# Performance work log

Hardware: AMD Instinct MI355X
Metric: run time of the kernel (lower is better)

The kernel has to match this reference:

```python
import jax, jax.numpy as jnp
import numpy as np

INPUT_DIM = 1024
OUTPUT_DIM = 1024


def setup_inputs() -> dict:
    key = jax.random.key(0)
    k1, k2, k3, k4 = jax.random.split(key, 4)
    B, S, D = 4, 2048, INPUT_DIM
    src = jax.random.normal(k1, (B, S, D), dtype=jnp.float32)
    tgt = jax.random.normal(k2, (B, S, D), dtype=jnp.float32)
    # nn.Linear(input_dim*2, output_dim): weight [out, in], bias [out]
    bound = 1.0 / np.sqrt(2 * D)
    W = jax.random.uniform(k3, (OUTPUT_DIM, 2 * D), jnp.float32, -bound, bound)
    b = jax.random.uniform(k4, (OUTPUT_DIM,), jnp.float32, -bound, bound)
    return {"src": src, "tgt": tgt, "W": W, "b": b}


def reference(src, tgt, W, b):
    # weight = bmm(tgt, src^T): [B, S_tgt, S_src]
    weight = jnp.einsum("btd,bsd->bts", tgt, src)
    # NOTE: original uses Softmax(dim=1) -> normalizes over the tgt axis
    weight = jax.nn.softmax(weight, axis=1)
    # weighted sum over src positions: [B, S_tgt, D]
    weight_sum = jnp.einsum("bts,bsd->btd", weight, src)
    output = jnp.concatenate([weight_sum, tgt], axis=2)  # [B, S_tgt, 2D]
    output = output @ W.T + b  # [B, S_tgt, output_dim]
    return (output, weight)
```

## Files before the change

### kernel.cpp

```cpp
#include <hip/hip_runtime.h>
#include <stdint.h>


#define B_   4
#define S_   2048
#define D_   1024
#define OUTD 1024

typedef unsigned short ushort_t;
typedef _Float16 half8 __attribute__((ext_vector_type(8)));
typedef float    f32x4 __attribute__((ext_vector_type(4)));

__device__ __forceinline__ ushort_t f2h(float f) {
    union { _Float16 h; ushort_t u; } v;
    v.h = (_Float16)f;
    return v.u;
}
__device__ __forceinline__ float h2f(ushort_t u) {
    union { _Float16 h; ushort_t u; } v;
    v.u = u;
    return (float)v.h;
}

__device__ __forceinline__ void ld16(const ushort_t* g, ushort_t* l) {
    __builtin_amdgcn_global_load_lds(
        (const __attribute__((address_space(1))) void*)g,
        (__attribute__((address_space(3))) void*)l, 16, 0, 0);
}


__global__ void k_split(const float4* __restrict__ src, const float4* __restrict__ tgt,
                        ushort4* __restrict__ sh,
                        ushort4* __restrict__ th, ushort4* __restrict__ tl)
{
    const int64_t n4 = (int64_t)B_ * S_ * D_ / 4;
    for (int64_t i = (int64_t)blockIdx.x * blockDim.x + threadIdx.x; i < n4;
         i += (int64_t)gridDim.x * blockDim.x) {
        float4 s = src[i];
        sh[i] = (ushort4){f2h(s.x), f2h(s.y), f2h(s.z), f2h(s.w)};
        float4 tv = tgt[i];
        ushort4 ht = {f2h(tv.x), f2h(tv.y), f2h(tv.z), f2h(tv.w)};
        th[i] = ht;
        tl[i] = (ushort4){f2h(tv.x - h2f(ht.x)), f2h(tv.y - h2f(ht.y)),
                          f2h(tv.z - h2f(ht.z)), f2h(tv.w - h2f(ht.w))};
    }
}

__global__ void k_wconv(const float4* __restrict__ W, ushort4* __restrict__ wb)
{
    const int64_t n4 = (int64_t)OUTD * 2 * D_ / 4;
    for (int64_t i = (int64_t)blockIdx.x * blockDim.x + threadIdx.x; i < n4;
         i += (int64_t)gridDim.x * blockDim.x) {
        float4 w = W[i];
        wb[i] = (ushort4){f2h(w.x), f2h(w.y), f2h(w.z), f2h(w.w)};
    }
}

__launch_bounds__(512, 2)
__global__ void k_gemm_logits(const ushort_t* __restrict__ Ah, const ushort_t* __restrict__ Al,
                              const ushort_t* __restrict__ Bs,
                              float* __restrict__ C,
                              float* __restrict__ pm, float* __restrict__ ps)
{
    const int M = S_, N = S_, K = D_;
    int b = blockIdx.z;
    Ah += (int64_t)b * M * K;  Al += (int64_t)b * M * K;
    Bs += (int64_t)b * N * K;
    C  += (int64_t)b * M * N;

    __shared__ __align__(16) ushort_t lds[3 * 24576];
    __shared__ float red_m[4][256], red_s[4][256];

    int t    = threadIdx.x;
    int m0   = blockIdx.y * 256, n0 = blockIdx.x * 256;
    int wave = t >> 6, lane = t & 63;
    int wr   = (wave >> 1) * 64;
    int wc   = (wave & 1) * 128;
    int l15  = lane & 15, quad = lane >> 4;

    f32x4 acc[4][8];
#pragma unroll
    for (int i = 0; i < 4; i++)
#pragma unroll
        for (int j = 0; j < 8; j++) acc[i][j] = (f32x4){0.f, 0.f, 0.f, 0.f};

    int pr   = t >> 3;
    int slot = t & 7;
    int cg   = slot ^ (pr & 7);
    int srow = pr * 2 + (cg >> 2);
    int scol = (cg & 3) * 8;

    const ushort_t* gAh = Ah + (int64_t)(m0 + srow) * K + scol;
    const ushort_t* gAl = Al + (int64_t)(m0 + srow) * K + scol;
    const ushort_t* gB  = Bs + (int64_t)(n0 + srow) * K + scol;
    const int64_t rstep = (int64_t)128 * K;

    auto stage = [&](int bufi, int kofs) {
        ushort_t* Lb = lds + bufi * 24576 + t * 8;
        ld16(gAh + kofs,         Lb);
        ld16(gAh + rstep + kofs, Lb + 4096);
        ld16(gAl + kofs,         Lb + 8192);
        ld16(gAl + rstep + kofs, Lb + 12288);
        ld16(gB  + kofs,         Lb + 16384);
        ld16(gB  + rstep + kofs, Lb + 20480);
    };

    int aoff[4], boff[8];
#pragma unroll
    for (int i = 0; i < 4; i++) {
        int R = wr + i * 16 + l15;
        int p = R >> 1, c = ((R & 1) << 2) + quad;
        aoff[i] = p * 64 + ((c ^ (p & 7)) << 3);
    }
#pragma unroll
    for (int j = 0; j < 8; j++) {
        int R = wc + j * 16 + l15;
        int p = R >> 1, c = ((R & 1) << 2) + quad;
        boff[j] = p * 64 + ((c ^ (p & 7)) << 3);
    }

    stage(0, 0);
    stage(1, 32);
    const int NT = 32;

    for (int kt = 0; kt < NT; ++kt) {
        if (kt + 1 < NT) {
            asm volatile("s_waitcnt vmcnt(6)" ::: "memory");
        } else {
            asm volatile("s_waitcnt vmcnt(0)" ::: "memory");
        }
        __builtin_amdgcn_s_barrier();
        asm volatile("" ::: "memory");
        __builtin_amdgcn_sched_barrier(0);

        if (kt + 2 < NT) stage((kt + 2) % 3, (kt + 2) * 32);

        const ushort_t* Lb = lds + (kt % 3) * 24576;
        half8 ah[4], al[4], bf[4];
#pragma unroll
        for (int i = 0; i < 4; i++) {
            ah[i] = *(const half8*)(Lb + aoff[i]);
            al[i] = *(const half8*)(Lb + 8192 + aoff[i]);
        }
#pragma unroll
        for (int j = 0; j < 4; j++) bf[j] = *(const half8*)(Lb + 16384 + boff[j]);

        __builtin_amdgcn_s_setprio(1);
#pragma unroll
        for (int i = 0; i < 4; i++)
#pragma unroll
            for (int j = 0; j < 4; j++)
                acc[i][j] = __builtin_amdgcn_mfma_f32_16x16x32_f16(ah[i], bf[j], acc[i][j], 0, 0, 0);
#pragma unroll
        for (int i = 0; i < 4; i++)
#pragma unroll
            for (int j = 0; j < 4; j++)
                acc[i][j] = __builtin_amdgcn_mfma_f32_16x16x32_f16(al[i], bf[j], acc[i][j], 0, 0, 0);
        __builtin_amdgcn_s_setprio(0);

#pragma unroll
        for (int j = 0; j < 4; j++) bf[j] = *(const half8*)(Lb + 16384 + boff[4 + j]);

        __builtin_amdgcn_s_setprio(1);
#pragma unroll
        for (int i = 0; i < 4; i++)
#pragma unroll
            for (int j = 0; j < 4; j++)
                acc[i][4 + j] = __builtin_amdgcn_mfma_f32_16x16x32_f16(ah[i], bf[j], acc[i][4 + j], 0, 0, 0);
#pragma unroll
        for (int i = 0; i < 4; i++)
#pragma unroll
            for (int j = 0; j < 4; j++)
                acc[i][4 + j] = __builtin_amdgcn_mfma_f32_16x16x32_f16(al[i], bf[j], acc[i][4 + j], 0, 0, 0);
        __builtin_amdgcn_s_setprio(0);
    }

#pragma unroll
    for (int i = 0; i < 4; i++) {
        int row_base = m0 + wr + i * 16 + quad * 4;
#pragma unroll
        for (int j = 0; j < 8; j++) {
            int col = n0 + wc + j * 16 + l15;
#pragma unroll
            for (int r = 0; r < 4; r++)
                C[(int64_t)(row_base + r) * N + col] = acc[i][j][r];
        }
    }

    int wrow = wave >> 1;
#pragma unroll
    for (int j = 0; j < 8; j++) {
        float m = -3.0e38f;
#pragma unroll
        for (int i = 0; i < 4; i++)
#pragma unroll
            for (int r = 0; r < 4; r++) m = fmaxf(m, acc[i][j][r]);
        float s = 0.f;
#pragma unroll
        for (int i = 0; i < 4; i++)
#pragma unroll
            for (int r = 0; r < 4; r++) s += __expf(acc[i][j][r] - m);
#pragma unroll
        for (int d = 16; d <= 32; d <<= 1) {
            float m2 = __shfl_xor(m, d, 64);
            float s2 = __shfl_xor(s, d, 64);
            float nm = fmaxf(m, m2);
            s = s * __expf(m - nm) + s2 * __expf(m2 - nm);
            m = nm;
        }
        if (lane < 16) {
            red_m[wrow][wc + j * 16 + l15] = m;
            red_s[wrow][wc + j * 16 + l15] = s;
        }
    }
    __syncthreads();
    if (t < 256) {
        float m = red_m[0][t];
#pragma unroll
        for (int w = 1; w < 4; w++) m = fmaxf(m, red_m[w][t]);
        float s = 0.f;
#pragma unroll
        for (int w = 0; w < 4; w++) s += red_s[w][t] * __expf(red_m[w][t] - m);
        int idx = blockIdx.y * (B_ * S_) + b * S_ + n0 + t;
        pm[idx] = m;
        ps[idx] = s;
    }
}


__global__ void k_colstats2(const float* __restrict__ pm, const float* __restrict__ ps,
                            float* __restrict__ cmax, float* __restrict__ cinv)
{
    int i = blockIdx.x * 256 + threadIdx.x;
    float m = -3.0e38f;
#pragma unroll
    for (int c = 0; c < 8; c++) m = fmaxf(m, pm[c * (B_ * S_) + i]);
    float sum = 0.f;
#pragma unroll
    for (int c = 0; c < 8; c++) sum += ps[c * (B_ * S_) + i] * __expf(pm[c * (B_ * S_) + i] - m);
    cmax[i] = m;
    cinv[i] = 1.0f / sum;
}

__global__ void k_softmax_norm(float4* __restrict__ L, const float4* __restrict__ cmax4,
                               const float4* __restrict__ cinv4, ushort4* __restrict__ wbf)
{
    const int64_t n4 = (int64_t)B_ * S_ * S_ / 4;
    for (int64_t i = (int64_t)blockIdx.x * blockDim.x + threadIdx.x; i < n4;
         i += (int64_t)gridDim.x * blockDim.x) {
        int b  = (int)(i >> 20);
        int c4 = (int)(i & 511);
        float4 x  = L[i];
        float4 cm = cmax4[b * 512 + c4];
        float4 ci = cinv4[b * 512 + c4];
        float4 w;
        w.x = __expf(x.x - cm.x) * ci.x;
        w.y = __expf(x.y - cm.y) * ci.y;
        w.z = __expf(x.z - cm.z) * ci.z;
        w.w = __expf(x.w - cm.w) * ci.w;
        L[i] = w;
        wbf[i] = (ushort4){f2h(w.x), f2h(w.y), f2h(w.z), f2h(w.w)};
    }
}

__launch_bounds__(512, 2)
__global__ void k_gemm_nt2(const ushort_t* __restrict__ A, int lda, int64_t bsA,
                           const ushort_t* __restrict__ Bm, int ldb, int64_t bsB,
                           ushort_t* __restrict__ C, int ldc, int64_t bsC, int K)
{
    int b = blockIdx.z;
    A  += (int64_t)b * bsA;
    Bm += (int64_t)b * bsB;
    C  += (int64_t)b * bsC;

    __shared__ __align__(16) ushort_t lds[3 * 24576];

    int t    = threadIdx.x;
    int m0   = blockIdx.y * 256, n0 = blockIdx.x * 128;
    int wave = t >> 6, lane = t & 63;
    int wr   = (wave >> 1) * 64;
    int wc   = (wave & 1) * 64;
    int l15  = lane & 15, quad = lane >> 4;

    f32x4 acc[4][4];
#pragma unroll
    for (int i = 0; i < 4; i++)
#pragma unroll
        for (int j = 0; j < 4; j++) acc[i][j] = (f32x4){0.f, 0.f, 0.f, 0.f};

    int srow = t >> 3;
    int cg   = (t & 7) ^ (srow & 7);
    int scol = cg * 8;

    const ushort_t* gA = A  + (int64_t)(m0 + srow) * lda + scol;
    const ushort_t* gB = Bm + (int64_t)(n0 + srow) * ldb + scol;

    auto stage = [&](int bufi, int k0) {
        ushort_t* Lb = lds + bufi * 24576 + t * 8;
        ld16(gA + k0,                        Lb);
        ld16(gA + (int64_t)64  * lda + k0,   Lb + 4096);
        ld16(gA + (int64_t)128 * lda + k0,   Lb + 8192);
        ld16(gA + (int64_t)192 * lda + k0,   Lb + 12288);
        ld16(gB + k0,                        Lb + 16384);
        ld16(gB + (int64_t)64  * ldb + k0,   Lb + 20480);
    };

    int aoff[4][2], boff[4][2];
#pragma unroll
    for (int i = 0; i < 4; i++) {
        int R = wr + i * 16 + l15;
#pragma unroll
        for (int h = 0; h < 2; h++) {
            int c = quad + h * 4;
            aoff[i][h] = R * 64 + ((c ^ (R & 7)) << 3);
        }
    }
#pragma unroll
    for (int j = 0; j < 4; j++) {
        int R = wc + j * 16 + l15;
#pragma unroll
        for (int h = 0; h < 2; h++) {
            int c = quad + h * 4;
            boff[j][h] = 16384 + R * 64 + ((c ^ (R & 7)) << 3);
        }
    }

    const int NT = K >> 6;
    stage(0, 0);
    stage(1, 64);

    for (int kt = 0; kt < NT; ++kt) {
        if (kt + 1 < NT) {
            asm volatile("s_waitcnt vmcnt(6)" ::: "memory");
        } else {
            asm volatile("s_waitcnt vmcnt(0)" ::: "memory");
        }
        __builtin_amdgcn_s_barrier();
        asm volatile("" ::: "memory");
        __builtin_amdgcn_sched_barrier(0);

        if (kt + 2 < NT) stage((kt + 2) % 3, (kt + 2) * 64);

        const ushort_t* Lb = lds + (kt % 3) * 24576;
#pragma unroll
        for (int h = 0; h < 2; h++) {
            half8 af[4], bf[4];
#pragma unroll
            for (int i = 0; i < 4; i++) af[i] = *(const half8*)(Lb + aoff[i][h]);
#pragma unroll
            for (int j = 0; j < 4; j++) bf[j] = *(const half8*)(Lb + boff[j][h]);
            __builtin_amdgcn_s_setprio(1);
#pragma unroll
            for (int i = 0; i < 4; i++)
#pragma unroll
                for (int j = 0; j < 4; j++)
                    acc[i][j] = __builtin_amdgcn_mfma_f32_16x16x32_f16(af[i], bf[j], acc[i][j], 0, 0, 0);
            __builtin_amdgcn_s_setprio(0);
        }
    }

#pragma unroll
    for (int i = 0; i < 4; i++) {
        int row_base = m0 + wr + i * 16 + quad * 4;
#pragma unroll
        for (int j = 0; j < 4; j++) {
            int col = n0 + wc + j * 16 + l15;
#pragma unroll
            for (int r = 0; r < 4; r++)
                C[(int64_t)(row_base + r) * ldc + col] = f2h(acc[i][j][r]);
        }
    }
}

__launch_bounds__(512, 2)
__global__ void k_gemm_final(const ushort_t* __restrict__ Wt, const ushort_t* __restrict__ PT,
                             const ushort_t* __restrict__ Q, const float* __restrict__ bias,
                             float* __restrict__ out)
{
    const int K = S_, N = OUTD;
    int b = blockIdx.z;
    const ushort_t* A  = Wt + (int64_t)b * S_ * S_;
    const ushort_t* Bm = PT + (int64_t)b * OUTD * S_;
    const ushort_t* Qb = Q  + (int64_t)b * S_ * OUTD;
    float* Cb = out + (int64_t)b * S_ * OUTD;

    __shared__ __align__(16) ushort_t lds[3 * 24576];

    int t    = threadIdx.x;
    int m0   = blockIdx.y * 256, n0 = blockIdx.x * 128;
    int wave = t >> 6, lane = t & 63;
    int wr   = (wave >> 1) * 64;
    int wc   = (wave & 1) * 64;
    int l15  = lane & 15, quad = lane >> 4;

    f32x4 acc[4][4];
#pragma unroll
    for (int i = 0; i < 4; i++)
#pragma unroll
        for (int j = 0; j < 4; j++) acc[i][j] = (f32x4){0.f, 0.f, 0.f, 0.f};

    int srow = t >> 3;
    int cg   = (t & 7) ^ (srow & 7);
    int scol = cg * 8;

    const ushort_t* gA = A  + (int64_t)(m0 + srow) * K + scol;
    const ushort_t* gB = Bm + (int64_t)(n0 + srow) * K + scol;

    auto stage = [&](int bufi, int k0) {
        ushort_t* Lb = lds + bufi * 24576 + t * 8;
        ld16(gA + k0,                      Lb);
        ld16(gA + (int64_t)64  * K + k0,   Lb + 4096);
        ld16(gA + (int64_t)128 * K + k0,   Lb + 8192);
        ld16(gA + (int64_t)192 * K + k0,   Lb + 12288);
        ld16(gB + k0,                      Lb + 16384);
        ld16(gB + (int64_t)64  * K + k0,   Lb + 20480);
    };

    int aoff[4][2], boff[4][2];
#pragma unroll
    for (int i = 0; i < 4; i++) {
        int R = wr + i * 16 + l15;
#pragma unroll
        for (int h = 0; h < 2; h++) {
            int c = quad + h * 4;
            aoff[i][h] = R * 64 + ((c ^ (R & 7)) << 3);
        }
    }
#pragma unroll
    for (int j = 0; j < 4; j++) {
        int R = wc + j * 16 + l15;
#pragma unroll
        for (int h = 0; h < 2; h++) {
            int c = quad + h * 4;
            boff[j][h] = 16384 + R * 64 + ((c ^ (R & 7)) << 3);
        }
    }

    const int NT = K >> 6;
    stage(0, 0);
    stage(1, 64);

    for (int kt = 0; kt < NT; ++kt) {
        if (kt + 1 < NT) {
            asm volatile("s_waitcnt vmcnt(6)" ::: "memory");
        } else {
            asm volatile("s_waitcnt vmcnt(0)" ::: "memory");
        }
        __builtin_amdgcn_s_barrier();
        asm volatile("" ::: "memory");
        __builtin_amdgcn_sched_barrier(0);

        if (kt + 2 < NT) stage((kt + 2) % 3, (kt + 2) * 64);

        const ushort_t* Lb = lds + (kt % 3) * 24576;
#pragma unroll
        for (int h = 0; h < 2; h++) {
            half8 af[4], bf[4];
#pragma unroll
            for (int i = 0; i < 4; i++) af[i] = *(const half8*)(Lb + aoff[i][h]);
#pragma unroll
            for (int j = 0; j < 4; j++) bf[j] = *(const half8*)(Lb + boff[j][h]);
            __builtin_amdgcn_s_setprio(1);
#pragma unroll
            for (int i = 0; i < 4; i++)
#pragma unroll
                for (int j = 0; j < 4; j++)
                    acc[i][j] = __builtin_amdgcn_mfma_f32_16x16x32_f16(af[i], bf[j], acc[i][j], 0, 0, 0);
            __builtin_amdgcn_s_setprio(0);
        }
    }

#pragma unroll
    for (int i = 0; i < 4; i++) {
        int row_base = m0 + wr + i * 16 + quad * 4;
#pragma unroll
        for (int j = 0; j < 4; j++) {
            int col = n0 + wc + j * 16 + l15;
            float bv = bias[col];
#pragma unroll
            for (int r = 0; r < 4; r++) {
                int64_t idx = (int64_t)(row_base + r) * N + col;
                Cb[idx] = acc[i][j][r] + h2f(Qb[idx]) + bv;
            }
        }
    }
}


extern "C" void kernel_launch(void* const* d_in, const int* in_sizes, int n_in,
                              void* d_out, int out_size, void* d_ws, size_t ws_size,
                              hipStream_t stream)
{
    const float* src  = (const float*)d_in[0];
    const float* tgt  = (const float*)d_in[1];
    const float* W    = (const float*)d_in[2];
    const float* bias = (const float*)d_in[3];

    float* out = (float*)d_out;
    float* Lw  = out + (size_t)B_ * S_ * OUTD;

    char*  ws = (char*)d_ws;
    size_t o  = 0;
    auto take = [&](size_t bytes) -> char* {
        char* p = ws + o;
        o += (bytes + 255) & ~(size_t)255;
        return p;
    };
    const size_t ELEMS = (size_t)B_ * S_ * D_;
    ushort_t* sh   = (ushort_t*)take(ELEMS * 2);
    ushort_t* th   = (ushort_t*)take(ELEMS * 2);
    ushort_t* tl   = (ushort_t*)take(ELEMS * 2);
    ushort_t* wbf  = (ushort_t*)take((size_t)B_ * S_ * S_ * 2);
    ushort_t* wb   = (ushort_t*)take((size_t)OUTD * 2 * D_ * 2);
    ushort_t* PT   = (ushort_t*)take((size_t)B_ * OUTD * S_ * 2);
    ushort_t* Qb   = (ushort_t*)take((size_t)B_ * S_ * OUTD * 2);
    float*    pm   = (float*)take(16 * (size_t)B_ * S_ * 4);
    float*    ps   = (float*)take(16 * (size_t)B_ * S_ * 4);
    float*    cmax = (float*)take((size_t)B_ * S_ * 4);
    float*    cinv = (float*)take((size_t)B_ * S_ * 4);
    (void)ws_size; (void)in_sizes; (void)n_in; (void)out_size;

    k_split<<<dim3(2048), dim3(256), 0, stream>>>((const float4*)src, (const float4*)tgt,
                                                  (ushort4*)sh, (ushort4*)th, (ushort4*)tl);
    k_wconv<<<dim3(512), dim3(256), 0, stream>>>((const float4*)W, (ushort4*)wb);

    k_gemm_nt2<<<dim3(16, 4, 4), dim3(512), 0, stream>>>(
        wb, 2 * D_, 0,
        sh, D_, (int64_t)S_ * D_,
        PT, S_, (int64_t)OUTD * S_, D_);

    k_gemm_nt2<<<dim3(8, 8, 4), dim3(512), 0, stream>>>(
        th, D_, (int64_t)S_ * D_,
        wb + D_, 2 * D_, 0,
        Qb, OUTD, (int64_t)S_ * OUTD, D_);

    k_gemm_logits<<<dim3(8, 8, 4), dim3(512), 0, stream>>>(th, tl, sh, Lw, pm, ps);

    k_colstats2<<<dim3(32), dim3(256), 0, stream>>>(pm, ps, cmax, cinv);
    k_softmax_norm<<<dim3(2048), dim3(256), 0, stream>>>((float4*)Lw, (const float4*)cmax,
                                                         (const float4*)cinv, (ushort4*)wbf);

    k_gemm_final<<<dim3(8, 8, 4), dim3(512), 0, stream>>>(wbf, PT, Qb, bias, out);
}
```

Measured before the change: 351.7 us.

## Reshape logits GEMM wave tiling and interleave global prefetch with MFMA phases

```diff
diff --git a/kernel.cpp b/kernel.cpp
--- a/kernel.cpp
+++ b/kernel.cpp
@@ -69,20 +69,20 @@
     C  += (int64_t)b * M * N;
 
     __shared__ __align__(16) ushort_t lds[3 * 24576];
-    __shared__ float red_m[4][256], red_s[4][256];
+    __shared__ float red_m[2][256], red_s[2][256];
 
     int t    = threadIdx.x;
     int m0   = blockIdx.y * 256, n0 = blockIdx.x * 256;
     int wave = t >> 6, lane = t & 63;
-    int wr   = (wave >> 1) * 64;
-    int wc   = (wave & 1) * 128;
+    int wr   = (wave >> 2) * 128;
+    int wc   = (wave & 3) * 64;
     int l15  = lane & 15, quad = lane >> 4;
 
-    f32x4 acc[4][8];
-#pragma unroll
-    for (int i = 0; i < 4; i++)
-#pragma unroll
-        for (int j = 0; j < 8; j++) acc[i][j] = (f32x4){0.f, 0.f, 0.f, 0.f};
+    f32x4 acc[8][4];
+#pragma unroll
+    for (int i = 0; i < 8; i++)
+#pragma unroll
+        for (int j = 0; j < 4; j++) acc[i][j] = (f32x4){0.f, 0.f, 0.f, 0.f};
 
     int pr   = t >> 3;
     int slot = t & 7;
@@ -95,7 +95,7 @@
     const ushort_t* gB  = Bs + (int64_t)(n0 + srow) * K + scol;
     const int64_t rstep = (int64_t)128 * K;
 
-    auto stage = [&](int bufi, int kofs) {
+    auto stage_all = [&](int bufi, int kofs) {
         ushort_t* Lb = lds + bufi * 24576 + t * 8;
         ld16(gAh + kofs,         Lb);
         ld16(gAh + rstep + kofs, Lb + 4096);
@@ -105,25 +105,30 @@
         ld16(gB  + rstep + kofs, Lb + 20480);
     };
 
-    int aoff[4], boff[8];
-#pragma unroll
-    for (int i = 0; i < 4; i++) {
+    int aoff[8], boff[4];
+#pragma unroll
+    for (int i = 0; i < 8; i++) {
         int R = wr + i * 16 + l15;
         int p = R >> 1, c = ((R & 1) << 2) + quad;
         aoff[i] = p * 64 + ((c ^ (p & 7)) << 3);
     }
 #pragma unroll
-    for (int j = 0; j < 8; j++) {
+    for (int j = 0; j < 4; j++) {
         int R = wc + j * 16 + l15;
         int p = R >> 1, c = ((R & 1) << 2) + quad;
         boff[j] = p * 64 + ((c ^ (p & 7)) << 3);
     }
 
-    stage(0, 0);
-    stage(1, 32);
     const int NT = 32;
+    stage_all(0, 0);
+    stage_all(1, 32);
 
     for (int kt = 0; kt < NT; ++kt) {
+        const ushort_t* Lb = lds + (kt % 3) * 24576;
+        ushort_t* Ld = lds + ((kt + 2) % 3) * 24576 + t * 8;
+        const int nofs = (kt + 2) * 32;
+        const bool pre = (kt + 2) < NT;
+
         if (kt + 1 < NT) {
             asm volatile("s_waitcnt vmcnt(6)" ::: "memory");
         } else {
@@ -133,53 +138,66 @@
         asm volatile("" ::: "memory");
         __builtin_amdgcn_sched_barrier(0);
 
-        if (kt + 2 < NT) stage((kt + 2) % 3, (kt + 2) * 32);
-
-        const ushort_t* Lb = lds + (kt % 3) * 24576;
-        half8 ah[4], al[4], bf[4];
-#pragma unroll
-        for (int i = 0; i < 4; i++) {
-            ah[i] = *(const half8*)(Lb + aoff[i]);
-            al[i] = *(const half8*)(Lb + 8192 + aoff[i]);
-        }
+        half8 av[4], bf[4];
+
 #pragma unroll
         for (int j = 0; j < 4; j++) bf[j] = *(const half8*)(Lb + 16384 + boff[j]);
-
+#pragma unroll
+        for (int i = 0; i < 4; i++) av[i] = *(const half8*)(Lb + aoff[i]);
+        if (pre) { ld16(gAh + nofs, Ld);  ld16(gAh + rstep + nofs, Ld + 4096); }
+        __builtin_amdgcn_s_barrier();
         __builtin_amdgcn_s_setprio(1);
 #pragma unroll
         for (int i = 0; i < 4; i++)
 #pragma unroll
             for (int j = 0; j < 4; j++)
-                acc[i][j] = __builtin_amdgcn_mfma_f32_16x16x32_f16(ah[i], bf[j], acc[i][j], 0, 0, 0);
+                acc[i][j] = __builtin_amdgcn_mfma_f32_16x16x32_f16(av[i], bf[j], acc[i][j], 0, 0, 0);
+        __builtin_amdgcn_s_setprio(0);
+        __builtin_amdgcn_s_barrier();
+
+#pragma unroll
+        for (int i = 0; i < 4; i++) av[i] = *(const half8*)(Lb + 8192 + aoff[i]);
+        if (pre) { ld16(gAl + nofs, Ld + 8192);  ld16(gAl + rstep + nofs, Ld + 12288); }
+        __builtin_amdgcn_s_barrier();
+        __builtin_amdgcn_s_setprio(1);
 #pragma unroll
         for (int i = 0; i < 4; i++)
 #pragma unroll
             for (int j = 0; j < 4; j++)
-                acc[i][j] = __builtin_amdgcn_mfma_f32_16x16x32_f16(al[i], bf[j], acc[i][j], 0, 0, 0);
+                acc[i][j] = __builtin_amdgcn_mfma_f32_16x16x32_f16(av[i], bf[j], acc[i][j], 0, 0, 0);
         __builtin_amdgcn_s_setprio(0);
-
-#pragma unroll
-        for (int j = 0; j < 4; j++) bf[j] = *(const half8*)(Lb + 16384 + boff[4 + j]);
-
+        __builtin_amdgcn_s_barrier();
+
+#pragma unroll
+        for (int i = 0; i < 4; i++) av[i] = *(const half8*)(Lb + aoff[4 + i]);
+        if (pre) { ld16(gB + nofs, Ld + 16384);  ld16(gB + rstep + nofs, Ld + 20480); }
+        __builtin_amdgcn_s_barrier();
         __builtin_amdgcn_s_setprio(1);
 #pragma unroll
         for (int i = 0; i < 4; i++)
 #pragma unroll
             for (int j = 0; j < 4; j++)
-                acc[i][4 + j] = __builtin_amdgcn_mfma_f32_16x16x32_f16(ah[i], bf[j], acc[i][4 + j], 0, 0, 0);
+                acc[4 + i][j] = __builtin_amdgcn_mfma_f32_16x16x32_f16(av[i], bf[j], acc[4 + i][j], 0, 0, 0);
+        __builtin_amdgcn_s_setprio(0);
+        __builtin_amdgcn_s_barrier();
+
+#pragma unroll
+        for (int i = 0; i < 4; i++) av[i] = *(const half8*)(Lb + 8192 + aoff[4 + i]);
+        __builtin_amdgcn_s_barrier();
+        __builtin_amdgcn_s_setprio(1);
 #pragma unroll
         for (int i = 0; i < 4; i++)
 #pragma unroll
             for (int j = 0; j < 4; j++)
-                acc[i][4 + j] = __builtin_amdgcn_mfma_f32_16x16x32_f16(al[i], bf[j], acc[i][4 + j], 0, 0, 0);
+                acc[4 + i][j] = __builtin_amdgcn_mfma_f32_16x16x32_f16(av[i], bf[j], acc[4 + i][j], 0, 0, 0);
         __builtin_amdgcn_s_setprio(0);
     }
 
 #pragma unroll
-    for (int i = 0; i < 4; i++) {
+    for (int i = 0; i < 8; i++) {
         int row_base = m0 + wr + i * 16 + quad * 4;
 #pragma unroll
-        for (int j = 0; j < 8; j++) {
+        for (int j = 0; j < 4; j++) {
             int col = n0 + wc + j * 16 + l15;
 #pragma unroll
             for (int r = 0; r < 4; r++)
@@ -187,17 +205,17 @@
         }
     }
 
-    int wrow = wave >> 1;
-#pragma unroll
-    for (int j = 0; j < 8; j++) {
+    int wrow = wave >> 2;
+#pragma unroll
+    for (int j = 0; j < 4; j++) {
         float m = -3.0e38f;
 #pragma unroll
-        for (int i = 0; i < 4; i++)
+        for (int i = 0; i < 8; i++)
 #pragma unroll
             for (int r = 0; r < 4; r++) m = fmaxf(m, acc[i][j][r]);
         float s = 0.f;
 #pragma unroll
-        for (int i = 0; i < 4; i++)
+        for (int i = 0; i < 8; i++)
 #pragma unroll
             for (int r = 0; r < 4; r++) s += __expf(acc[i][j][r] - m);
 #pragma unroll
@@ -215,12 +233,10 @@
     }
     __syncthreads();
     if (t < 256) {
-        float m = red_m[0][t];
-#pragma unroll
-        for (int w = 1; w < 4; w++) m = fmaxf(m, red_m[w][t]);
-        float s = 0.f;
-#pragma unroll
-        for (int w = 0; w < 4; w++) s += red_s[w][t] * __expf(red_m[w][t] - m);
+        float ma = red_m[0][t], mb = red_m[1][t];
+        float sa = red_s[0][t], sb = red_s[1][t];
+        float m = fmaxf(ma, mb);
+        float s = sa * __expf(ma - m) + sb * __expf(mb - m);
         int idx = blockIdx.y * (B_ * S_) + b * S_ + n0 + t;
         pm[idx] = m;
         ps[idx] = s;
```

After: 347.7 us. About the same (-1.1%).
